# Performance work log

Measured on AMD Instinct MI355X. Metric: run time of the kernel, lower is better.

## Reference

```python
import jax, jax.numpy as jnp
import numpy as np

C_RGB, CR = 64, 64
B, H, W = 4, 256, 256
EPS = 1e-6


def conv1x1(x, w, b):
    # x: [B,Cin,H,W], w: [Cout,Cin], b: [Cout]
    return jnp.einsum('bchw,oc->bohw', x, w) + b[None, :, None, None]


def layernorm2d(x, w, b):
    # LayerNorm over channel dim per pixel (NAFNet LayerNorm2d)
    mu = jnp.mean(x, axis=1, keepdims=True)
    var = jnp.var(x, axis=1, keepdims=True)
    xn = (x - mu) / jnp.sqrt(var + EPS)
    return xn * w[None, :, None, None] + b[None, :, None, None]


def setup_inputs() -> dict:
    key = jax.random.key(0)
    ks = jax.random.split(key, 16)
    c2 = C_RGB // 2
    s1 = 1.0 / np.sqrt(C_RGB)
    s2 = 1.0 / np.sqrt(CR)
    return {
        'x_rgb': jax.random.normal(ks[0], (B, C_RGB, H, W), jnp.float32),
        'x_hfw': jax.random.normal(ks[1], (B, CR, H, W), jnp.float32),
        'ln_w': jnp.ones((C_RGB,), jnp.float32),
        'ln_b': jnp.zeros((C_RGB,), jnp.float32),
        'w_l1': jax.random.normal(ks[2], (C_RGB, C_RGB), jnp.float32) * s1,
        'b_l1': jnp.zeros((C_RGB,), jnp.float32),
        'w_r1': jax.random.normal(ks[3], (C_RGB, CR), jnp.float32) * s2,
        'b_r1': jnp.zeros((C_RGB,), jnp.float32),
        'w_l2': jax.random.normal(ks[4], (c2, C_RGB), jnp.float32) * s1,
        'b_l2': jnp.zeros((c2,), jnp.float32),
        'w_r2': jax.random.normal(ks[5], (c2, CR), jnp.float32) * s2,
        'b_r2': jnp.zeros((c2,), jnp.float32),
        'w_lres': jax.random.normal(ks[6], (c2, C_RGB), jnp.float32) * s1,
        'b_lres': jnp.zeros((c2,), jnp.float32),
        'w_rres': jax.random.normal(ks[7], (c2, CR), jnp.float32) * s2,
        'b_rres': jnp.zeros((c2,), jnp.float32),
        'beta': jnp.zeros((1, c2, 1, 1), jnp.float32),
        'gamma': jnp.zeros((1, c2, 1, 1), jnp.float32),
    }


def reference(x_rgb, x_hfw, ln_w, ln_b, w_l1, b_l1, w_r1, b_r1, w_l2, b_l2,
              w_r2, b_r2, w_lres, b_lres, w_rres, b_rres, beta, gamma):
    scale = (0.5 * (C_RGB + CR)) ** (-0.5)
    # Projections; keep [B,C,H,W] layout then einsum over the needed axes
    q_l = conv1x1(layernorm2d(x_rgb, ln_w, ln_b), w_l1, b_l1)  # [B,c,H,W]
    q_r = conv1x1(x_hfw, w_r1, b_r1)                            # [B,c,H,W]
    v_l = conv1x1(x_rgb, w_l2, b_l2)                            # [B,c2,H,W]
    v_r = conv1x1(x_hfw, w_r2, b_r2)                            # [B,c2,H,W]
    # Attention per row: [B,H,W(left),W(right)]
    attn = jnp.einsum('bchw,bchv->bhwv', q_l, q_r) * scale
    # r2l: softmax over right-width, contract with V_r -> [B,H,W,c2]
    f_r2l = jnp.einsum('bhwv,bchv->bhwc', jax.nn.softmax(attn, axis=-1), v_r)
    # l2r: softmax over left-width of transposed attn, contract with V_l -> [B,H,W,c2]
    f_l2r = jnp.einsum('bhvw,bchw->bhvc',
                       jax.nn.softmax(jnp.swapaxes(attn, -1, -2), axis=-1), v_l)
    f_r2l = jnp.transpose(f_r2l, (0, 3, 1, 2)) * beta   # [B,c2,H,W]
    f_l2r = jnp.transpose(f_l2r, (0, 3, 1, 2)) * gamma  # [B,c2,H,W]
    out_l = conv1x1(x_rgb, w_lres, b_lres) + f_r2l
    out_r = conv1x1(x_hfw, w_rres, b_rres) + f_l2r
    return jnp.concatenate((out_l, out_r), axis=1)
```

## Files before the change

kernel.cpp:

```cpp
#include <hip/hip_runtime.h>
#include <hip/hip_bf16.h>

#define HW 65536

typedef short short8 __attribute__((ext_vector_type(8)));
typedef float f32x4 __attribute__((ext_vector_type(4)));

__device__ __forceinline__ unsigned short f2bf(float x) {
    return __builtin_bit_cast(unsigned short, __float2bfloat16(x));
}
__device__ __forceinline__ f32x4 mfma16(short8 a, short8 b, f32x4 c) {
    return __builtin_amdgcn_mfma_f32_16x16x32_bf16(a, b, c, 0, 0, 0);
}
__device__ __forceinline__ short8 packw8(const float* w) {
    const float4 a = *(const float4*)w;
    const float4 b = *(const float4*)(w + 4);
    uint4 u;
    u.x = f2bf(a.x) | ((unsigned)f2bf(a.y) << 16);
    u.y = f2bf(a.z) | ((unsigned)f2bf(a.w) << 16);
    u.z = f2bf(b.x) | ((unsigned)f2bf(b.y) << 16);
    u.w = f2bf(b.z) | ((unsigned)f2bf(b.w) << 16);
    return __builtin_bit_cast(short8, u);
}

__global__ __launch_bounds__(512, 3) void res_kernel(
    const float* __restrict__ xg_l, const float* __restrict__ xg_r,
    const float* __restrict__ wlres, const float* __restrict__ blres,
    const float* __restrict__ wrres, const float* __restrict__ brres,
    float* __restrict__ out)
{
    __shared__ __align__(16) uint4 X16[2048];

    const int bh = blockIdx.x;
    const int b = bh >> 8, h = bh & 255;
    const int tid = threadIdx.x;
    const int wv = tid >> 6, lane = tid & 63;
    const int g = lane >> 4, lr = lane & 15;
    const int px = tid & 255, half = tid >> 8;

    const size_t obase = (size_t)b * 64 * HW + (size_t)h * 256;

    for (int side = 0; side < 2; ++side) {
        const float* xg = side ? xg_r : xg_l;
        const float* W  = side ? wrres : wlres;
        const float* Bz = side ? brres : blres;

        const float* xp = xg + obase + px;
#pragma unroll
        for (int cb = 0; cb < 4; ++cb) {
            const int ch = half * 32 + cb * 8;
            float v[8];
#pragma unroll
            for (int k = 0; k < 8; ++k) v[k] = xp[(size_t)(ch + k) * HW];
            uint4 u;
            u.x = f2bf(v[0]) | ((unsigned)f2bf(v[1]) << 16);
            u.y = f2bf(v[2]) | ((unsigned)f2bf(v[3]) << 16);
            u.z = f2bf(v[4]) | ((unsigned)f2bf(v[5]) << 16);
            u.w = f2bf(v[6]) | ((unsigned)f2bf(v[7]) << 16);
            X16[px * 8 + ((half * 4 + cb) ^ (px & 7))] = u;
        }
        __syncthreads();

        short8 bfr0[2], bfr1[2];
#pragma unroll
        for (int i = 0; i < 2; ++i) {
            const int p = (wv * 2 + i) * 16 + lr;
            bfr0[i] = __builtin_bit_cast(short8, X16[p * 8 + (g ^ (p & 7))]);
            bfr1[i] = __builtin_bit_cast(short8, X16[p * 8 + ((4 + g) ^ (p & 7))]);
        }
#pragma unroll
        for (int ot = 0; ot < 2; ++ot) {
            const int out0 = ot * 16;
            short8 af0 = packw8(&W[(out0 + lr) * 64 + 8 * g]);
            short8 af1 = packw8(&W[(out0 + lr) * 64 + 32 + 8 * g]);
            const int ch0 = out0 + 4 * g;
            const f32x4 bz = *(const f32x4*)&Bz[ch0];
#pragma unroll
            for (int i = 0; i < 2; ++i) {
                f32x4 acc = {0.f, 0.f, 0.f, 0.f};
                acc = mfma16(af0, bfr0[i], acc);
                acc = mfma16(af1, bfr1[i], acc);
                const int p = (wv * 2 + i) * 16 + lr;
                float* op = out + obase + p + (size_t)(side * 32 + ch0) * HW;
#pragma unroll
                for (int r = 0; r < 4; ++r) op[(size_t)r * HW] = acc[r] + bz[r];
            }
        }
        __syncthreads();
    }
}

__global__ __launch_bounds__(256) void prep_kernel(
    const float* __restrict__ wl1, const float* __restrict__ bl1,
    const float* __restrict__ wr1,
    const float* __restrict__ wl2, const float* __restrict__ wr2,
    const float* __restrict__ lnw, const float* __restrict__ lnb,
    __hip_bfloat16* __restrict__ wpack, float* __restrict__ st)
{
    const int tid = threadIdx.x;
    if (tid < 64) {
        const int o = tid;
        float s = 0.f, t = 0.f;
        for (int c = 0; c < 64; ++c) {
            __hip_bfloat16 wb = __float2bfloat16(wl1[o*64+c] * lnw[c]);
            wpack[o*64+c] = wb;
            s += __bfloat162float(wb);
            t += wl1[o*64+c] * lnb[c];
        }
        st[o] = s;
        st[64+o] = t + bl1[o];
    } else if (tid < 128) {
        const int o = tid - 64;
        for (int c = 0; c < 64; ++c) wpack[4096 + o*64+c] = __float2bfloat16(wr1[o*64+c]);
    } else if (tid < 160) {
        const int o = tid - 128;
        for (int c = 0; c < 64; ++c) wpack[8192 + o*64+c] = __float2bfloat16(wl2[o*64+c]);
    } else if (tid < 192) {
        const int o = tid - 160;
        for (int c = 0; c < 64; ++c) wpack[10240 + o*64+c] = __float2bfloat16(wr2[o*64+c]);
    }
}

#define QL_OFF 0
#define QR_OFF 32768
#define VL_OFF 65536
#define VR_OFF 81920
#define XP_OFF 98304
#define AUX_OFF 131072
#define SMEM_BYTES (131072 + 7680)

__global__ __launch_bounds__(512, 2) void attn_kernel(
    const float* __restrict__ xg_l, const float* __restrict__ xg_r,
    const __hip_bfloat16* __restrict__ wpack, const float* __restrict__ st,
    const float* __restrict__ bqr_g, const float* __restrict__ bl2,
    const float* __restrict__ br2, const float* __restrict__ beta,
    const float* __restrict__ gamma, float* __restrict__ out)
{
    __shared__ __align__(16) unsigned char smem[SMEM_BYTES];
    __shared__ int sNeed[2];

    const int tid = threadIdx.x;
    float* coefA = (float*)(smem + AUX_OFF + 3328);

    if (tid < 64) {
        const float cf = tid < 32 ? beta[tid] : gamma[tid - 32];
        coefA[tid] = cf;
        unsigned long long m = __ballot(cf != 0.f);
        if (tid == 0) {
            sNeed[0] = (unsigned)(m & 0xffffffffull) ? 1 : 0;
            sNeed[1] = (unsigned)(m >> 32)           ? 1 : 0;
        }
    }
    __syncthreads();
    const bool needL = sNeed[0] != 0;
    const bool needR = sNeed[1] != 0;
    if (!(needL || needR)) return;

    const int bh = blockIdx.x;
    const int b = bh >> 8, h = bh & 255;
    const int wv = tid >> 6, lane = tid & 63;
    const int g = lane >> 4, lr = lane & 15;
    const int px = tid & 255, half = tid >> 8;

    float* aArr  = (float*)(smem + AUX_OFF);
    float* bbArr = (float*)(smem + AUX_OFF + 1024);
    float* sArr  = (float*)(smem + AUX_OFF + 2048);
    float* tArr  = (float*)(smem + AUX_OFF + 2304);
    float* bqrA  = (float*)(smem + AUX_OFF + 2560);
    float* bvA   = (float*)(smem + AUX_OFF + 2816);
    float* pS    = (float*)(smem + AUX_OFF + 3584);
    float* pQ    = (float*)(smem + AUX_OFF + 5632);

    const size_t obase = (size_t)b * 64 * HW + (size_t)h * 256;
    const size_t xbase = obase + px;

    float xl[32], xr_[32];
#pragma unroll
    for (int c = 0; c < 32; ++c) xl[c] = xg_l[xbase + (size_t)(half*32 + c) * HW];
#pragma unroll
    for (int c = 0; c < 32; ++c) xr_[c] = xg_r[xbase + (size_t)(half*32 + c) * HW];

    if (tid < 64) {
        sArr[tid] = st[tid];
        tArr[tid] = st[64 + tid];
        bqrA[tid] = bqr_g[tid];
        bvA[tid]  = tid < 32 ? bl2[tid] : br2[tid - 32];
    }

    {
        float s = 0.f, q = 0.f;
#pragma unroll
        for (int c = 0; c < 32; ++c) { s += xl[c]; q = fmaf(xl[c], xl[c], q); }
        pS[half*256 + px] = s;
        pQ[half*256 + px] = q;
    }

    uint4* X16 = (uint4*)(smem + XP_OFF);
#pragma unroll
    for (int cb = 0; cb < 4; ++cb) {
        uint4 u;
        u.x = f2bf(xl[cb*8+0]) | ((unsigned)f2bf(xl[cb*8+1]) << 16);
        u.y = f2bf(xl[cb*8+2]) | ((unsigned)f2bf(xl[cb*8+3]) << 16);
        u.z = f2bf(xl[cb*8+4]) | ((unsigned)f2bf(xl[cb*8+5]) << 16);
        u.w = f2bf(xl[cb*8+6]) | ((unsigned)f2bf(xl[cb*8+7]) << 16);
        X16[px*8 + ((half*4 + cb) ^ (px & 7))] = u;
    }
    __syncthreads();
    if (half == 0) {
        float s = pS[px] + pS[256 + px];
        float q = pQ[px] + pQ[256 + px];
        float mu = s * (1.f / 64.f);
        float var = q * (1.f / 64.f) - mu * mu;
        float rstd = rsqrtf(var + 1e-6f);
        aArr[px] = rstd;
        bbArr[px] = -rstd * mu;
    }
    __syncthreads();

    const uint4* W16 = (const uint4*)wpack;

    auto proj_side = [&](int wq, int wvv, unsigned char* qdst,
                         unsigned char* vdst, int chbase, bool ln, bool doV) {
        short8 bfr0[2], bfr1[2];
#pragma unroll
        for (int i = 0; i < 2; ++i) {
            int p = (wv*2 + i)*16 + lr;
            bfr0[i] = __builtin_bit_cast(short8, X16[p*8 + (g ^ (p&7))]);
            bfr1[i] = __builtin_bit_cast(short8, X16[p*8 + ((4+g) ^ (p&7))]);
        }
#pragma unroll
        for (int ot = 0; ot < 4; ++ot) {
            const int out0 = ot * 16;
            short8 af0 = __builtin_bit_cast(short8, W16[wq + (out0+lr)*8 + g]);
            short8 af1 = __builtin_bit_cast(short8, W16[wq + (out0+lr)*8 + 4 + g]);
            const int ch0 = out0 + 4*g;
            f32x4 c1 = *(const f32x4*)&(ln ? sArr : bqrA)[ch0];
            f32x4 c2 = ln ? *(const f32x4*)&tArr[ch0] : (f32x4){0.f,0.f,0.f,0.f};
#pragma unroll
            for (int i = 0; i < 2; ++i) {
                f32x4 acc = {0.f,0.f,0.f,0.f};
                acc = mfma16(af0, bfr0[i], acc);
                acc = mfma16(af1, bfr1[i], acc);
                const int p = (wv*2+i)*16 + lr;
                float q0,q1,q2,q3;
                if (ln) {
                    const float a_ = aArr[p], b_ = bbArr[p];
                    q0 = fmaf(a_, acc[0], fmaf(b_, c1[0], c2[0]));
                    q1 = fmaf(a_, acc[1], fmaf(b_, c1[1], c2[1]));
                    q2 = fmaf(a_, acc[2], fmaf(b_, c1[2], c2[2]));
                    q3 = fmaf(a_, acc[3], fmaf(b_, c1[3], c2[3]));
                } else {
                    q0 = acc[0]+c1[0]; q1 = acc[1]+c1[1];
                    q2 = acc[2]+c1[2]; q3 = acc[3]+c1[3];
                }
                unsigned lo = f2bf(q0) | ((unsigned)f2bf(q1) << 16);
                unsigned hi = f2bf(q2) | ((unsigned)f2bf(q3) << 16);
                *(uint2*)(qdst + p*128 + (((ch0>>3) ^ (p&7))*16) + (ch0&7)*2)
                    = make_uint2(lo, hi);
            }
        }
        if (doV) {
#pragma unroll
            for (int ot = 0; ot < 2; ++ot) {
                const int out0 = ot * 16;
                short8 af0 = __builtin_bit_cast(short8, W16[wvv + (out0+lr)*8 + g]);
                short8 af1 = __builtin_bit_cast(short8, W16[wvv + (out0+lr)*8 + 4 + g]);
                const int ch = out0 + lr;
                const float bv = bvA[chbase + ch];
#pragma unroll
                for (int i = 0; i < 2; ++i) {
                    f32x4 acc = {0.f,0.f,0.f,0.f};
                    acc = mfma16(bfr0[i], af0, acc);
                    acc = mfma16(bfr1[i], af1, acc);
                    unsigned lo = f2bf(acc[0]+bv) | ((unsigned)f2bf(acc[1]+bv) << 16);
                    unsigned hi = f2bf(acc[2]+bv) | ((unsigned)f2bf(acc[3]+bv) << 16);
                    const int vb = (wv*2+i)*2 + (g>>1);
                    *(uint2*)(vdst + ch*512 + ((vb ^ (ch&7))*16) + (g&1)*8)
                        = make_uint2(lo, hi);
                }
            }
        }
    };

    proj_side(0, 1024, smem + QL_OFF, smem + VL_OFF, 0, true, needR);
    __syncthreads();

#pragma unroll
    for (int cb = 0; cb < 4; ++cb) {
        uint4 u;
        u.x = f2bf(xr_[cb*8+0]) | ((unsigned)f2bf(xr_[cb*8+1]) << 16);
        u.y = f2bf(xr_[cb*8+2]) | ((unsigned)f2bf(xr_[cb*8+3]) << 16);
        u.z = f2bf(xr_[cb*8+4]) | ((unsigned)f2bf(xr_[cb*8+5]) << 16);
        u.w = f2bf(xr_[cb*8+6]) | ((unsigned)f2bf(xr_[cb*8+7]) << 16);
        X16[px*8 + ((half*4 + cb) ^ (px & 7))] = u;
    }
    __syncthreads();

    proj_side(512, 1280, smem + QR_OFF, smem + VR_OFF, 32, false, needL);
    __syncthreads();

    const int dir = wv >> 2, wsub = wv & 3;
    if (dir ? needR : needL) {
        unsigned char* Pw = smem + XP_OFF + wv * 4096;
        const float cs = 0.125f * 1.44269504088896f;

        const uint4* Q16 = (const uint4*)(smem + (dir ? QR_OFF : QL_OFF));
        const uint4* K16 = (const uint4*)(smem + (dir ? QL_OFF : QR_OFF));
        const uint4* V16 = (const uint4*)(smem + (dir ? VL_OFF : VR_OFF));
        const float* coef = coefA + dir * 32;

        for (int c = 0; c < 4; ++c) {
            const int row0 = c * 64 + wsub * 16;
            const int qpx = row0 + lr;
            short8 qf0 = __builtin_bit_cast(short8, Q16[qpx*8 + (g ^ (qpx&7))]);
            short8 qf1 = __builtin_bit_cast(short8, Q16[qpx*8 + ((4+g) ^ (qpx&7))]);

            f32x4 sacc[16];
#pragma unroll
            for (int t = 0; t < 16; ++t) sacc[t] = (f32x4){0.f,0.f,0.f,0.f};
            __builtin_amdgcn_s_setprio(1);
#pragma unroll
            for (int t = 0; t < 16; ++t) {
                const int key = t * 16 + lr;
                const int sw = key & 7;
                short8 a0 = __builtin_bit_cast(short8, K16[key*8 + (g ^ sw)]);
                short8 a1 = __builtin_bit_cast(short8, K16[key*8 + ((4+g) ^ sw)]);
                sacc[t] = mfma16(a0, qf0, sacc[t]);
                sacc[t] = mfma16(a1, qf1, sacc[t]);
            }
            __builtin_amdgcn_s_setprio(0);
            float mx = -3.0e38f;
#pragma unroll
            for (int t = 0; t < 16; ++t)
                mx = fmaxf(mx, fmaxf(fmaxf(sacc[t][0], sacc[t][1]),
                                     fmaxf(sacc[t][2], sacc[t][3])));
            mx = fmaxf(mx, __shfl_xor(mx, 16));
            mx = fmaxf(mx, __shfl_xor(mx, 32));

            float lsum = 0.f;
            f32x4 o0 = (f32x4){0.f,0.f,0.f,0.f};
            f32x4 o1 = (f32x4){0.f,0.f,0.f,0.f};
#pragma unroll
            for (int hh = 0; hh < 2; ++hh) {
#pragma unroll
                for (int t8 = 0; t8 < 8; ++t8) {
                    const int t16 = hh * 8 + t8;
                    float p0 = exp2f((sacc[t16][0] - mx) * cs);
                    float p1 = exp2f((sacc[t16][1] - mx) * cs);
                    float p2 = exp2f((sacc[t16][2] - mx) * cs);
                    float p3 = exp2f((sacc[t16][3] - mx) * cs);
                    lsum += (p0 + p1) + (p2 + p3);
                    unsigned lo = f2bf(p0) | ((unsigned)f2bf(p1) << 16);
                    unsigned hi = f2bf(p2) | ((unsigned)f2bf(p3) << 16);
                    int pb = (2*t8 + (g >> 1)) ^ (lr & 7);
                    *(uint2*)(Pw + lr*256 + pb*16 + (g & 1)*8) = make_uint2(lo, hi);
                }
#pragma unroll
                for (int t = 0; t < 4; ++t) {
                    const int pb = 4*t + g;
                    const int vb = 16*hh + 4*t + g;
                    short8 pa = __builtin_bit_cast(short8,
                                *(const uint4*)(Pw + lr*256 + ((pb ^ (lr&7))*16)));
                    short8 v0 = __builtin_bit_cast(short8, V16[lr*32 + (vb ^ (lr&7))]);
                    short8 v1 = __builtin_bit_cast(short8, V16[(16+lr)*32 + (vb ^ (lr&7))]);
                    o0 = mfma16(pa, v0, o0);
                    o1 = mfma16(pa, v1, o1);
                }
            }
            lsum += __shfl_xor(lsum, 16);
            lsum += __shfl_xor(lsum, 32);
            const float inv = 1.f / lsum;

            float* Ot = (float*)Pw;
#pragma unroll
            for (int r = 0; r < 4; ++r) Ot[lr*17 + (g*4 + r)] = o0[r];
#pragma unroll
            for (int r = 0; r < 4; ++r) Ot[(16+lr)*17 + (g*4 + r)] = o1[r];

            float* outp = out + obase + (size_t)(dir*32) * HW + row0 + lr;
#pragma unroll
            for (int it = 0; it < 8; ++it) {
                const int ch = it*4 + g;
                outp[(size_t)ch * HW] += Ot[ch*17 + lr] * inv * coef[ch];
            }
        }
    }
}

extern "C" void kernel_launch(void* const* d_in, const int* in_sizes, int n_in,
                              void* d_out, int out_size, void* d_ws, size_t ws_size,
                              hipStream_t stream) {
    (void)in_sizes; (void)n_in; (void)out_size; (void)ws_size;
    const float* xr    = (const float*)d_in[0];
    const float* xh    = (const float*)d_in[1];
    const float* lnw   = (const float*)d_in[2];
    const float* lnb   = (const float*)d_in[3];
    const float* wl1   = (const float*)d_in[4];
    const float* bl1   = (const float*)d_in[5];
    const float* wr1   = (const float*)d_in[6];
    const float* br1   = (const float*)d_in[7];
    const float* wl2   = (const float*)d_in[8];
    const float* bl2   = (const float*)d_in[9];
    const float* wr2   = (const float*)d_in[10];
    const float* br2   = (const float*)d_in[11];
    const float* wlres = (const float*)d_in[12];
    const float* blres = (const float*)d_in[13];
    const float* wrres = (const float*)d_in[14];
    const float* brres = (const float*)d_in[15];
    const float* beta  = (const float*)d_in[16];
    const float* gamma = (const float*)d_in[17];
    float* out = (float*)d_out;

    __hip_bfloat16* wpack = (__hip_bfloat16*)d_ws;
    float* st = (float*)((unsigned char*)d_ws + 32768);

    res_kernel<<<dim3(1024), dim3(512), 0, stream>>>(
        xr, xh, wlres, blres, wrres, brres, out);
    prep_kernel<<<dim3(1), dim3(256), 0, stream>>>(
        wl1, bl1, wr1, wl2, wr2, lnw, lnb, wpack, st);
    attn_kernel<<<dim3(1024), dim3(512), 0, stream>>>(
        xr, xh, wpack, st, br1, bl2, br2, beta, gamma, out);
}
```

Before: 50.52 us.

## Split residual conv by side into grid dimension and drop LDS staging

```diff
diff --git a/kernel.cpp b/kernel.cpp
--- a/kernel.cpp
+++ b/kernel.cpp
@@ -23,70 +23,65 @@
     return __builtin_bit_cast(short8, u);
 }
 
-__global__ __launch_bounds__(512, 3) void res_kernel(
+__global__ __launch_bounds__(256, 8) void res_kernel(
     const float* __restrict__ xg_l, const float* __restrict__ xg_r,
     const float* __restrict__ wlres, const float* __restrict__ blres,
     const float* __restrict__ wrres, const float* __restrict__ brres,
     float* __restrict__ out)
 {
-    __shared__ __align__(16) uint4 X16[2048];
-
     const int bh = blockIdx.x;
+    const int side = blockIdx.y;
     const int b = bh >> 8, h = bh & 255;
     const int tid = threadIdx.x;
     const int wv = tid >> 6, lane = tid & 63;
     const int g = lane >> 4, lr = lane & 15;
-    const int px = tid & 255, half = tid >> 8;
+
+    const float* xg = side ? xg_r : xg_l;
+    const float* W  = side ? wrres : wlres;
+    const float* Bz = side ? brres : blres;
 
     const size_t obase = (size_t)b * 64 * HW + (size_t)h * 256;
-
-    for (int side = 0; side < 2; ++side) {
-        const float* xg = side ? xg_r : xg_l;
-        const float* W  = side ? wrres : wlres;
-        const float* Bz = side ? brres : blres;
-
-        const float* xp = xg + obase + px;
-#pragma unroll
-        for (int cb = 0; cb < 4; ++cb) {
-            const int ch = half * 32 + cb * 8;
-            float v[8];
-#pragma unroll
-            for (int k = 0; k < 8; ++k) v[k] = xp[(size_t)(ch + k) * HW];
-            uint4 u;
-            u.x = f2bf(v[0]) | ((unsigned)f2bf(v[1]) << 16);
-            u.y = f2bf(v[2]) | ((unsigned)f2bf(v[3]) << 16);
-            u.z = f2bf(v[4]) | ((unsigned)f2bf(v[5]) << 16);
-            u.w = f2bf(v[6]) | ((unsigned)f2bf(v[7]) << 16);
-            X16[px * 8 + ((half * 4 + cb) ^ (px & 7))] = u;
-        }
-        __syncthreads();
-
-        short8 bfr0[2], bfr1[2];
-#pragma unroll
-        for (int i = 0; i < 2; ++i) {
-            const int p = (wv * 2 + i) * 16 + lr;
-            bfr0[i] = __builtin_bit_cast(short8, X16[p * 8 + (g ^ (p & 7))]);
-            bfr1[i] = __builtin_bit_cast(short8, X16[p * 8 + ((4 + g) ^ (p & 7))]);
-        }
+    float* outp = out + obase + (size_t)(side * 32) * HW;
+
+    short8 af[2][2];
+    f32x4 bz[2];
+#pragma unroll
+    for (int ot = 0; ot < 2; ++ot) {
+        af[ot][0] = packw8(&W[(ot * 16 + lr) * 64 + 8 * g]);
+        af[ot][1] = packw8(&W[(ot * 16 + lr) * 64 + 32 + 8 * g]);
+        bz[ot] = *(const f32x4*)&Bz[ot * 16 + 4 * g];
+    }
+
+#pragma unroll
+    for (int i = 0; i < 4; ++i) {
+        const int p = (wv * 4 + i) * 16 + lr;
+        const float* xp = xg + obase + p;
+        float v0[8], v1[8];
+#pragma unroll
+        for (int k = 0; k < 8; ++k) v0[k] = xp[(size_t)(8 * g + k) * HW];
+#pragma unroll
+        for (int k = 0; k < 8; ++k) v1[k] = xp[(size_t)(32 + 8 * g + k) * HW];
+        uint4 u0, u1;
+        u0.x = f2bf(v0[0]) | ((unsigned)f2bf(v0[1]) << 16);
+        u0.y = f2bf(v0[2]) | ((unsigned)f2bf(v0[3]) << 16);
+        u0.z = f2bf(v0[4]) | ((unsigned)f2bf(v0[5]) << 16);
+        u0.w = f2bf(v0[6]) | ((unsigned)f2bf(v0[7]) << 16);
+        u1.x = f2bf(v1[0]) | ((unsigned)f2bf(v1[1]) << 16);
+        u1.y = f2bf(v1[2]) | ((unsigned)f2bf(v1[3]) << 16);
+        u1.z = f2bf(v1[4]) | ((unsigned)f2bf(v1[5]) << 16);
+        u1.w = f2bf(v1[6]) | ((unsigned)f2bf(v1[7]) << 16);
+        const short8 xb0 = __builtin_bit_cast(short8, u0);
+        const short8 xb1 = __builtin_bit_cast(short8, u1);
+
 #pragma unroll
         for (int ot = 0; ot < 2; ++ot) {
-            const int out0 = ot * 16;
-            short8 af0 = packw8(&W[(out0 + lr) * 64 + 8 * g]);
-            short8 af1 = packw8(&W[(out0 + lr) * 64 + 32 + 8 * g]);
-            const int ch0 = out0 + 4 * g;
-            const f32x4 bz = *(const f32x4*)&Bz[ch0];
-#pragma unroll
-            for (int i = 0; i < 2; ++i) {
-                f32x4 acc = {0.f, 0.f, 0.f, 0.f};
-                acc = mfma16(af0, bfr0[i], acc);
-                acc = mfma16(af1, bfr1[i], acc);
-                const int p = (wv * 2 + i) * 16 + lr;
-                float* op = out + obase + p + (size_t)(side * 32 + ch0) * HW;
-#pragma unroll
-                for (int r = 0; r < 4; ++r) op[(size_t)r * HW] = acc[r] + bz[r];
-            }
-        }
-        __syncthreads();
+            f32x4 acc = {0.f, 0.f, 0.f, 0.f};
+            acc = mfma16(af[ot][0], xb0, acc);
+            acc = mfma16(af[ot][1], xb1, acc);
+            float* op = outp + p + (size_t)(ot * 16 + 4 * g) * HW;
+#pragma unroll
+            for (int r = 0; r < 4; ++r) op[(size_t)r * HW] = acc[r] + bz[ot][r];
+        }
     }
 }
 
@@ -414,7 +409,7 @@
     __hip_bfloat16* wpack = (__hip_bfloat16*)d_ws;
     float* st = (float*)((unsigned char*)d_ws + 32768);
 
-    res_kernel<<<dim3(1024), dim3(512), 0, stream>>>(
+    res_kernel<<<dim3(1024, 2), dim3(256), 0, stream>>>(
         xr, xh, wlres, blres, wrres, brres, out);
     prep_kernel<<<dim3(1), dim3(256), 0, stream>>>(
         wl1, bl1, wr1, wl2, wr2, lnw, lnb, wpack, st);
```

After: 78.01 us. +54.4%, slower.
